# Optimization experiments

Hardware: AMD Instinct MI355X
Metric: run time of the kernel (lower is better)

The kernel has to match this reference:

```python
import jax, jax.numpy as jnp
import numpy as np

N = 32768          # total nodes
B = 64             # graphs
NPG = N // B       # nodes per graph (equal-sized graphs)
E = 524288         # edges (before self-loops)
D_IN, HID, HEADS, D_OUT = 128, 64, 4, 128
DH = HID * HEADS   # 256
NEG_SLOPE = 0.2
EPS = 1e-5

def _leaky(x):
    return jnp.where(x >= 0, x, NEG_SLOPE * x)

def gat_conv(x, src, dst, W, a_src, a_dst, b, concat):
    """PyG-style GATConv (self-loops already included in src/dst)."""
    H, C = a_src.shape
    h = (x @ W).reshape(N, H, C)                       # [N,H,C]
    es = jnp.einsum('nhc,hc->nh', h, a_src)            # score from source feats
    ed = jnp.einsum('nhc,hc->nh', h, a_dst)            # score from target feats
    e = _leaky(es[src] + ed[dst])                      # [E',H]
    m = jax.ops.segment_max(e, dst, num_segments=N)    # stable softmax per dst
    p = jnp.exp(e - m[dst])
    s = jax.ops.segment_sum(p, dst, num_segments=N)
    alpha = p / s[dst]                                 # [E',H]
    out = jax.ops.segment_sum(h[src] * alpha[..., None], dst, num_segments=N)
    out = out.reshape(N, H * C) if concat else out.mean(axis=1)
    return out + b

def mha(x, Wi, bi, Wo, bo, heads):
    """torch.nn.MultiheadAttention (batch_first, no mask, eval)."""
    Bb, T, D = x.shape
    qkv = x @ Wi.T + bi                                # [B,T,3D]
    q, k, v = jnp.split(qkv, 3, axis=-1)
    hd = D // heads
    def sp(t):
        return t.reshape(Bb, T, heads, hd).transpose(0, 2, 1, 3)  # [B,h,T,hd]
    q, k, v = sp(q), sp(k), sp(v)
    scores = jnp.einsum('bhqd,bhkd->bhqk', q, k) / jnp.sqrt(jnp.float32(hd))
    attn = jax.nn.softmax(scores, axis=-1)
    o = jnp.einsum('bhqk,bhkd->bhqd', attn, v)
    o = o.transpose(0, 2, 1, 3).reshape(Bb, T, D)
    return o @ Wo.T + bo

def layer_norm(x, g, b):
    mu = x.mean(-1, keepdims=True)
    var = x.var(-1, keepdims=True)
    return (x - mu) / jnp.sqrt(var + EPS) * g + b

def setup_inputs() -> dict:
    key = jax.random.key(0)
    ks = jax.random.split(key, 20)
    s = 0.1
    inp = {
        'x': jax.random.normal(ks[0], (N, D_IN), jnp.float32),
        'edge_index': jax.random.randint(ks[1], (2, E), 0, N, jnp.int64),
        'batch': (jnp.arange(N, dtype=jnp.int64) // NPG),
        # gat1: D_IN -> HEADS*HID (concat)
        'W1': jax.random.normal(ks[2], (D_IN, HEADS * HID), jnp.float32) * s,
        'aS1': jax.random.normal(ks[3], (HEADS, HID), jnp.float32) * s,
        'aD1': jax.random.normal(ks[4], (HEADS, HID), jnp.float32) * s,
        'b1': jnp.zeros((HEADS * HID,), jnp.float32),
        # gat2: DH -> HEADS*HID (concat)
        'W2': jax.random.normal(ks[5], (DH, HEADS * HID), jnp.float32) * s,
        'aS2': jax.random.normal(ks[6], (HEADS, HID), jnp.float32) * s,
        'aD2': jax.random.normal(ks[7], (HEADS, HID), jnp.float32) * s,
        'b2': jnp.zeros((HEADS * HID,), jnp.float32),
        # gat3: DH -> D_OUT, heads=1, concat=False (mean)
        'W3': jax.random.normal(ks[8], (DH, D_OUT), jnp.float32) * s,
        'aS3': jax.random.normal(ks[9], (1, D_OUT), jnp.float32) * s,
        'aD3': jax.random.normal(ks[10], (1, D_OUT), jnp.float32) * s,
        'b3': jnp.zeros((D_OUT,), jnp.float32),
        # MultiheadAttention
        'Wi': jax.random.normal(ks[11], (3 * DH, DH), jnp.float32) * s,
        'bi': jnp.zeros((3 * DH,), jnp.float32),
        'Wo': jax.random.normal(ks[12], (DH, DH), jnp.float32) * s,
        'bo': jnp.zeros((DH,), jnp.float32),
        # LayerNorm
        'gamma': jnp.ones((DH,), jnp.float32),
        'beta': jnp.zeros((DH,), jnp.float32),
    }
    return inp

def reference(x, edge_index, batch, W1, aS1, aD1, b1, W2, aS2, aD2, b2,
              W3, aS3, aD3, b3, Wi, bi, Wo, bo, gamma, beta):
    # add self-loops (PyG GATConv default)
    loops = jnp.arange(N, dtype=edge_index.dtype)
    src = jnp.concatenate([edge_index[0], loops])
    dst = jnp.concatenate([edge_index[1], loops])

    x1 = jax.nn.elu(gat_conv(x, src, dst, W1, aS1, aD1, b1, concat=True))
    x2 = jax.nn.elu(gat_conv(x1, src, dst, W2, aS2, aD2, b2, concat=True))

    # ragged-to-dense batching: batch = arange(N)//NPG (equal-sized, sorted),
    # so the torch python loop reduces to a reshape with no padding.
    x2b = x2.reshape(B, NPG, DH)
    attended = mha(x2b, Wi, bi, Wo, bo, HEADS).reshape(N, DH)

    x2a = layer_norm(attended + x2, gamma, beta)
    x3 = gat_conv(x2a, src, dst, W3, aS3, aD3, b3, concat=False)
    return x3
```

## Files before the change

kernel.cpp:

```cpp
#include <hip/hip_runtime.h>

typedef _Float16 half_t;
typedef _Float16 half8  __attribute__((ext_vector_type(8)));
typedef _Float16 half4v __attribute__((ext_vector_type(4)));
typedef _Float16 half2v __attribute__((ext_vector_type(2)));
typedef float    f32x4  __attribute__((ext_vector_type(4)));
typedef float    f32x2  __attribute__((ext_vector_type(2)));

constexpr int N_NODES = 32768;
constexpr int NPG_    = 512;

#define MFMA16(a, b, c) __builtin_amdgcn_mfma_f32_16x16x32_f16((a), (b), (c), 0, 0, 0)

#if defined(__has_builtin)
#  if __has_builtin(__builtin_amdgcn_cvt_pk_f16_fp8)
#    define HAVE_PK_F16_FP8 1
#  else
#    define HAVE_PK_F16_FP8 0
#  endif
#else
#  define HAVE_PK_F16_FP8 0
#endif

__device__ __forceinline__ void gload_lds16(const half_t* g, half_t* l) {
  __builtin_amdgcn_global_load_lds(
      (const __attribute__((address_space(1))) void*)g,
      (__attribute__((address_space(3))) void*)l, 16, 0, 0);
}

__device__ __forceinline__ void fp8x4_fma(int wrd, half2v p, half2v* acc) {
#if HAVE_PK_F16_FP8
  half2v lo = __builtin_amdgcn_cvt_pk_f16_fp8((short)(wrd & 0xffff));
  half2v hi = __builtin_amdgcn_cvt_pk_f16_fp8((short)(((unsigned)wrd) >> 16));
#else
  f32x2 flo = __builtin_amdgcn_cvt_pk_f32_fp8(wrd, false);
  f32x2 fhi = __builtin_amdgcn_cvt_pk_f32_fp8(wrd, true);
  half2v lo = {(half_t)flo.x, (half_t)flo.y};
  half2v hi = {(half_t)fhi.x, (half_t)fhi.y};
#endif
  acc[0] += p * lo;
  acc[1] += p * hi;
}

__global__ void k_hist(const int* __restrict__ dst, int* __restrict__ deg, int E) {
  int i = blockIdx.x * 256 + threadIdx.x;
  if (i < E) atomicAdd(&deg[dst[i]], 1);
}

__global__ __launch_bounds__(256) void k_scan1(const int* __restrict__ deg,
                                               int* __restrict__ partial,
                                               int* __restrict__ blockSums) {
  __shared__ int sd[256];
  int t = threadIdx.x;
  int i = blockIdx.x * 256 + t;
  int v = deg[i];
  sd[t] = v;
  __syncthreads();
  int acc = v;
  for (int off = 1; off < 256; off <<= 1) {
    int add = (t >= off) ? sd[t - off] : 0;
    __syncthreads();
    acc += add;
    sd[t] = acc;
    __syncthreads();
  }
  partial[i] = acc - v;
  if (t == 255) blockSums[blockIdx.x] = acc;
}

__global__ __launch_bounds__(128) void k_scan2(const int* __restrict__ blockSums,
                                               int* __restrict__ blockOff,
                                               int* __restrict__ rowptr) {
  __shared__ int sd[128];
  int t = threadIdx.x;
  int v = blockSums[t];
  sd[t] = v;
  __syncthreads();
  for (int off = 1; off < 128; off <<= 1) {
    int add = (t >= off) ? sd[t - off] : 0;
    __syncthreads();
    sd[t] += add;
    __syncthreads();
  }
  blockOff[t] = sd[t] - v;
  if (t == 127) rowptr[N_NODES] = sd[t];
}

__global__ __launch_bounds__(256) void k_scan3(const int* __restrict__ partial,
                                               const int* __restrict__ blockOff,
                                               int* __restrict__ rowptr,
                                               int* __restrict__ fill,
                                               int* __restrict__ col) {
  int i = blockIdx.x * 256 + threadIdx.x;
  int rp = partial[i] + blockOff[blockIdx.x];
  rowptr[i] = rp;
  fill[i] = 1;
  col[rp] = i;
}

__global__ void k_scatter(const int* __restrict__ src, const int* __restrict__ dst,
                          const int* __restrict__ rowptr, int* __restrict__ fill,
                          int* __restrict__ col, int E) {
  int i = blockIdx.x * 256 + threadIdx.x;
  if (i < E) {
    int d = dst[i];
    int pos = rowptr[d] + atomicAdd(&fill[d], 1);
    col[pos] = src[i];
  }
}

__global__ void k_convert(
    const float* __restrict__ x,  half_t* __restrict__ x_h,
    const float* __restrict__ W1, half_t* __restrict__ W1t,
    const float* __restrict__ W2, half_t* __restrict__ W2t,
    const float* __restrict__ W3, half_t* __restrict__ W3t,
    const float* __restrict__ Wi, half_t* __restrict__ Wi_h,
    const float* __restrict__ Wo, half_t* __restrict__ Wo_h,
    int* __restrict__ deg)
{
  int bid = blockIdx.x, t = threadIdx.x;
  if (bid < 16384) {
    int i = bid * 256 + t;
    x_h[i] = (half_t)x[i];
  } else if (bid < 16512) {
    int i = (bid - 16384) * 256 + t;
    int o = i >> 7, k = i & 127;
    W1t[i] = (half_t)W1[k * 256 + o];
  } else if (bid < 16768) {
    int i = (bid - 16512) * 256 + t;
    int o = i >> 8, k = i & 255;
    W2t[i] = (half_t)W2[k * 256 + o];
  } else if (bid < 16896) {
    int i = (bid - 16768) * 256 + t;
    int o = i >> 8, k = i & 255;
    W3t[i] = (half_t)W3[k * 128 + o];
  } else if (bid < 17664) {
    int i = (bid - 16896) * 256 + t;
    Wi_h[i] = (half_t)Wi[i];
  } else if (bid < 17920) {
    int i = (bid - 17664) * 256 + t;
    Wo_h[i] = (half_t)Wo[i];
  } else {
    deg[(bid - 17920) * 256 + t] = 1;
  }
}

__device__ __forceinline__ void gemm_wide_body(
    int bx, int by,
    const half_t* __restrict__ A, const half_t* __restrict__ Bt,
    const float* __restrict__ bias, int bias_per_row,
    half_t* __restrict__ outh, int Nc, int K,
    half_t* As, half_t* Bs)
{
  int w = threadIdx.x >> 6, lane = threadIdx.x & 63;
  int r = lane & 15, q = lane >> 4;
  int m0 = by * 128, n0 = bx * 64;
  int mh = (w & 1) * 64, nh = (w >> 1) * 32;
  f32x4 acc[4][2];
  #pragma unroll
  for (int i = 0; i < 4; i++)
    #pragma unroll
    for (int j = 0; j < 2; j++) acc[i][j] = f32x4{0.f, 0.f, 0.f, 0.f};

  int srow = lane >> 3, sc = lane & 7;

  for (int k0 = 0; k0 < K; k0 += 64) {
    __syncthreads();
    #pragma unroll
    for (int i = 0; i < 4; i++) {
      int R0 = w * 32 + i * 8;
      int row = R0 + srow;
      int cg = sc ^ (row & 7);
      gload_lds16(A + (size_t)(m0 + row) * K + k0 + cg * 8, &As[R0 * 64]);
    }
    #pragma unroll
    for (int i = 0; i < 2; i++) {
      int R0 = w * 16 + i * 8;
      int row = R0 + srow;
      int cg = sc ^ (row & 7);
      gload_lds16(Bt + (size_t)(n0 + row) * K + k0 + cg * 8, &Bs[R0 * 64]);
    }
    __syncthreads();
    #pragma unroll
    for (int kk = 0; kk < 2; kk++) {
      half8 af[4], bf[2];
      #pragma unroll
      for (int t = 0; t < 4; t++) {
        int rr = mh + t * 16 + r;
        af[t] = *(const half8*)&As[rr * 64 + (((kk * 4 + q) ^ (rr & 7)) << 3)];
      }
      #pragma unroll
      for (int t = 0; t < 2; t++) {
        int rr = nh + t * 16 + r;
        bf[t] = *(const half8*)&Bs[rr * 64 + (((kk * 4 + q) ^ (rr & 7)) << 3)];
      }
      #pragma unroll
      for (int ti = 0; ti < 4; ti++)
        #pragma unroll
        for (int tj = 0; tj < 2; tj++)
          acc[ti][tj] = MFMA16(af[ti], bf[tj], acc[ti][tj]);
    }
  }

  #pragma unroll
  for (int tj = 0; tj < 2; tj++) {
    int colc = n0 + nh + tj * 16 + r;
    float bc = bias_per_row ? 0.f : bias[colc];
    #pragma unroll
    for (int ti = 0; ti < 4; ti++) {
      #pragma unroll
      for (int i = 0; i < 4; i++) {
        int row = m0 + mh + ti * 16 + q * 4 + i;
        float bv = bias_per_row ? bias[row] : bc;
        outh[(size_t)row * Nc + colc] = (half_t)(acc[ti][tj][i] + bv);
      }
    }
  }
}

__global__ __launch_bounds__(256) void k_gemm_qkv2(
    const half_t* __restrict__ x2, const half_t* __restrict__ Wi_h,
    const float* __restrict__ bi,
    half_t* __restrict__ qk, half_t* __restrict__ vt)
{
  __shared__ __align__(16) half_t As[128 * 64];
  __shared__ __align__(16) half_t Bs[64 * 64];
  int id = blockIdx.x;
  if (id < 2048) {
    gemm_wide_body(id & 7, id >> 3, x2, Wi_h, bi, 0, qk, 512, 256, As, Bs);
  } else {
    int id2 = id - 2048;
    gemm_wide_body(id2 & 511, id2 >> 9, Wi_h + 512 * 256, x2, bi + 512, 1,
                   vt, 32768, 256, As, Bs);
  }
}

template<int NC, int H, bool FP8O>
__global__ __launch_bounds__(256) void k_gemm_gat(
    const half_t* __restrict__ A, const half_t* __restrict__ Bt,
    half_t* __restrict__ outh, unsigned char* __restrict__ out8, int K,
    const float* __restrict__ aS, const float* __restrict__ aD,
    float* __restrict__ es, float* __restrict__ ed)
{
  __shared__ __align__(16) half_t As[128 * 64];
  __shared__ __align__(16) half_t Bs[64 * 64];
  __shared__ float sRed[2][4][64];
  int w = threadIdx.x >> 6, lane = threadIdx.x & 63;
  int cc = lane & 15, qq = lane >> 4;
  int m0 = blockIdx.y * 128, n0 = blockIdx.x * 64;
  int mh = (w & 1) * 64, nh = (w >> 1) * 32;
  f32x4 acc[4][2];
  #pragma unroll
  for (int i = 0; i < 4; i++)
    #pragma unroll
    for (int j = 0; j < 2; j++) acc[i][j] = f32x4{0.f, 0.f, 0.f, 0.f};

  int srow = lane >> 3, sc = lane & 7;

  for (int k0 = 0; k0 < K; k0 += 64) {
    __syncthreads();
    #pragma unroll
    for (int i = 0; i < 4; i++) {
      int R0 = w * 32 + i * 8;
      int row = R0 + srow;
      int cg = sc ^ (row & 7);
      gload_lds16(A + (size_t)(m0 + row) * K + k0 + cg * 8, &As[R0 * 64]);
    }
    #pragma unroll
    for (int i = 0; i < 2; i++) {
      int R0 = w * 16 + i * 8;
      int row = R0 + srow;
      int cg = sc ^ (row & 7);
      gload_lds16(Bt + (size_t)(n0 + row) * K + k0 + cg * 8, &Bs[R0 * 64]);
    }
    __syncthreads();
    #pragma unroll
    for (int kk = 0; kk < 2; kk++) {
      half8 af[4], bf[2];
      #pragma unroll
      for (int t = 0; t < 4; t++) {
        int rr = mh + t * 16 + cc;
        af[t] = *(const half8*)&As[rr * 64 + (((kk * 4 + qq) ^ (rr & 7)) << 3)];
      }
      #pragma unroll
      for (int t = 0; t < 2; t++) {
        int rr = nh + t * 16 + cc;
        bf[t] = *(const half8*)&Bs[rr * 64 + (((kk * 4 + qq) ^ (rr & 7)) << 3)];
      }
      #pragma unroll
      for (int ti = 0; ti < 4; ti++)
        #pragma unroll
        for (int tj = 0; tj < 2; tj++)
          acc[ti][tj] = MFMA16(af[ti], bf[tj], acc[ti][tj]);
    }
  }

  float aSv[2], aDv[2];
  #pragma unroll
  for (int tj = 0; tj < 2; tj++) {
    int colg = n0 + nh + tj * 16 + cc;
    aSv[tj] = aS[colg];
    aDv[tj] = aD[colg];
  }
  #pragma unroll
  for (int ti = 0; ti < 4; ti++) {
    #pragma unroll
    for (int i = 0; i < 4; i++) {
      int rloc = mh + ti * 16 + qq * 4 + i;
      float ps = 0.f, pd = 0.f;
      #pragma unroll
      for (int tj = 0; tj < 2; tj++) {
        int colg = n0 + nh + tj * 16 + cc;
        float v = acc[ti][tj][i];
        if (FP8O) {
          int pk = __builtin_amdgcn_cvt_pk_fp8_f32(v, v, 0, false);
          out8[(size_t)(m0 + rloc) * NC + colg] = (unsigned char)pk;
        } else {
          outh[(size_t)(m0 + rloc) * NC + colg] = (half_t)v;
        }
        ps += v * aSv[tj];
        pd += v * aDv[tj];
      }
      #pragma unroll
      for (int off = 1; off < 16; off <<= 1) {
        ps += __shfl_xor(ps, off);
        pd += __shfl_xor(pd, off);
      }
      if (cc == 0) {
        sRed[0][w][ti * 16 + qq * 4 + i] = ps;
        sRed[1][w][ti * 16 + qq * 4 + i] = pd;
      }
    }
  }
  __syncthreads();
  if (threadIdx.x < 128) {
    int row = threadIdx.x;
    int wlo = row >> 6, ri = row & 63;
    float ps = sRed[0][wlo][ri] + sRed[0][wlo + 2][ri];
    float pd = sRed[1][wlo][ri] + sRed[1][wlo + 2][ri];
    if (H == 4) {
      int head = n0 >> 6;
      es[(size_t)(m0 + row) * 4 + head] = ps;
      ed[(size_t)(m0 + row) * 4 + head] = pd;
    } else {
      atomicAdd(&es[m0 + row], ps);
      atomicAdd(&ed[m0 + row], pd);
    }
  }
}

__global__ __launch_bounds__(256) void k_gemm_ln(
    const half_t* __restrict__ A, const half_t* __restrict__ Bt,
    const float* __restrict__ bias, const half_t* __restrict__ res,
    const float* __restrict__ gamma, const float* __restrict__ beta,
    half_t* __restrict__ outh, float* __restrict__ es0, float* __restrict__ ed0)
{
  __shared__ __align__(16) half_t As[64 * 64];
  __shared__ __align__(16) half_t Bs[256 * 64];
  __shared__ float sSum[4][64], sSq[4][64];
  __shared__ float sMR[64][2];
  int w = threadIdx.x >> 6, lane = threadIdx.x & 63;
  int r = lane & 15, q = lane >> 4;
  int m0 = blockIdx.x * 64;
  int nh = w * 64;

  if (threadIdx.x < 64) es0[m0 + threadIdx.x] = 0.f;
  else if (threadIdx.x < 128) ed0[m0 + threadIdx.x - 64] = 0.f;

  f32x4 acc[4][4];
  #pragma unroll
  for (int i = 0; i < 4; i++)
    #pragma unroll
    for (int j = 0; j < 4; j++) acc[i][j] = f32x4{0.f, 0.f, 0.f, 0.f};

  int srow = lane >> 3, sc = lane & 7;

  for (int k0 = 0; k0 < 256; k0 += 64) {
    __syncthreads();
    #pragma unroll
    for (int i = 0; i < 2; i++) {
      int R0 = w * 16 + i * 8;
      int row = R0 + srow;
      int cg = sc ^ (row & 7);
      gload_lds16(A + (size_t)(m0 + row) * 256 + k0 + cg * 8, &As[R0 * 64]);
    }
    #pragma unroll
    for (int i = 0; i < 8; i++) {
      int R0 = w * 64 + i * 8;
      int row = R0 + srow;
      int cg = sc ^ (row & 7);
      gload_lds16(Bt + (size_t)row * 256 + k0 + cg * 8, &Bs[R0 * 64]);
    }
    __syncthreads();
    #pragma unroll
    for (int kk = 0; kk < 2; kk++) {
      half8 af[4], bf[4];
      #pragma unroll
      for (int t = 0; t < 4; t++) {
        int rr = t * 16 + r;
        af[t] = *(const half8*)&As[rr * 64 + (((kk * 4 + q) ^ (rr & 7)) << 3)];
      }
      #pragma unroll
      for (int t = 0; t < 4; t++) {
        int rr = nh + t * 16 + r;
        bf[t] = *(const half8*)&Bs[rr * 64 + (((kk * 4 + q) ^ (rr & 7)) << 3)];
      }
      #pragma unroll
      for (int ti = 0; ti < 4; ti++)
        #pragma unroll
        for (int tj = 0; tj < 4; tj++)
          acc[ti][tj] = MFMA16(af[ti], bf[tj], acc[ti][tj]);
    }
  }

  float gv[4], bv[4];
  #pragma unroll
  for (int tj = 0; tj < 4; tj++) {
    int col = nh + tj * 16 + r;
    gv[tj] = gamma[col];
    bv[tj] = beta[col];
  }
  #pragma unroll
  for (int ti = 0; ti < 4; ti++) {
    #pragma unroll
    for (int i = 0; i < 4; i++) {
      int row = ti * 16 + q * 4 + i;
      float s = 0.f, ss = 0.f;
      #pragma unroll
      for (int tj = 0; tj < 4; tj++) {
        int col = nh + tj * 16 + r;
        float v = acc[ti][tj][i] + bias[col]
                + (float)res[(size_t)(m0 + row) * 256 + col];
        acc[ti][tj][i] = v;
        s += v;
        ss += v * v;
      }
      #pragma unroll
      for (int off = 1; off < 16; off <<= 1) {
        s  += __shfl_xor(s, off);
        ss += __shfl_xor(ss, off);
      }
      if (r == 0) { sSum[w][row] = s; sSq[w][row] = ss; }
    }
  }
  __syncthreads();
  if (threadIdx.x < 64) {
    int row = threadIdx.x;
    float s  = sSum[0][row] + sSum[1][row] + sSum[2][row] + sSum[3][row];
    float ss = sSq[0][row] + sSq[1][row] + sSq[2][row] + sSq[3][row];
    float mean = s * (1.f / 256.f);
    float var  = ss * (1.f / 256.f) - mean * mean;
    sMR[row][0] = mean;
    sMR[row][1] = rsqrtf(var + 1e-5f);
  }
  __syncthreads();
  #pragma unroll
  for (int ti = 0; ti < 4; ti++) {
    #pragma unroll
    for (int i = 0; i < 4; i++) {
      int row = ti * 16 + q * 4 + i;
      float mean = sMR[row][0], rstd = sMR[row][1];
      #pragma unroll
      for (int tj = 0; tj < 4; tj++) {
        int col = nh + tj * 16 + r;
        outh[(size_t)(m0 + row) * 256 + col] =
            (half_t)((acc[ti][tj][i] - mean) * rstd * gv[tj] + bv[tj]);
      }
    }
  }
}

__global__ __launch_bounds__(256) void k_agg_f16(
    const half_t* __restrict__ h, const float* __restrict__ es,
    const float* __restrict__ ed, const float* __restrict__ bias,
    const int* __restrict__ rowptr, const int* __restrict__ col,
    half_t* __restrict__ outh)
{
  int lane = threadIdx.x & 63;
  int g = lane >> 4, li = lane & 15;
  int n = blockIdx.x * 4 + (threadIdx.x >> 6);
  int cbase = li * 16;
  int hl = li >> 2;
  float edn = ed[(size_t)n * 4 + hl];
  int j0 = rowptr[n], j1 = rowptr[n + 1];
  const half_t* hb = h + cbase;

  float sum0 = 0.f, sum1 = 0.f;
  half8 acc0[2], acc1[2];
  #pragma unroll
  for (int i = 0; i < 2; i++) {
    acc0[i] = half8{0, 0, 0, 0, 0, 0, 0, 0};
    acc1[i] = half8{0, 0, 0, 0, 0, 0, 0, 0};
  }
  for (int j = j0 + g; j < j1; j += 8) {
    int jb = j + 4;
    int s0 = col[j];
    int s1 = col[(jb < j1) ? jb : j];
    float e0 = es[(size_t)s0 * 4 + hl] + edn;
    e0 = fmaxf(e0, 0.2f * e0);
    float e1 = es[(size_t)s1 * 4 + hl] + edn;
    e1 = fmaxf(e1, 0.2f * e1);
    e1 = (jb < j1) ? e1 : -1e30f;
    const half_t* hp0 = hb + (size_t)s0 * 256;
    const half_t* hp1 = hb + (size_t)s1 * 256;
    float p0 = exp2f(e0 * 1.44269504f - 8.65617025f);
    float p1 = exp2f(e1 * 1.44269504f - 8.65617025f);
    sum0 += p0; sum1 += p1;
    half_t q0 = (half_t)p0, q1 = (half_t)p1;
    half8 pv0 = {q0, q0, q0, q0, q0, q0, q0, q0};
    half8 pv1 = {q1, q1, q1, q1, q1, q1, q1, q1};
    #pragma unroll
    for (int i = 0; i < 2; i++) {
      half8 v0 = *(const half8*)(hp0 + i * 8);
      half8 v1 = *(const half8*)(hp1 + i * 8);
      acc0[i] += pv0 * v0;
      acc1[i] += pv1 * v1;
    }
  }
  float sum = sum0 + sum1;
  sum += __shfl_xor(sum, 16);
  sum += __shfl_xor(sum, 32);
  float av[16];
  #pragma unroll
  for (int i = 0; i < 16; i++) {
    av[i] = (float)acc0[i >> 3][i & 7] + (float)acc1[i >> 3][i & 7];
    av[i] += __shfl_xor(av[i], 16);
    av[i] += __shfl_xor(av[i], 32);
  }
  float inv = 1.f / sum;
  if (g == 0) {
    size_t obase = (size_t)n * 256 + cbase;
    #pragma unroll
    for (int p8 = 0; p8 < 2; p8++) {
      half8 hv;
      #pragma unroll
      for (int i = 0; i < 8; i++) {
        float t = av[p8 * 8 + i] * inv + bias[cbase + p8 * 8 + i];
        t = (t > 0.f) ? t : __expf(t) - 1.f;
        hv[i] = (half_t)t;
      }
      *(half8*)(outh + obase + p8 * 8) = hv;
    }
  }
}

__global__ __launch_bounds__(256) void k_agg_fp8(
    const unsigned char* __restrict__ hq, const float* __restrict__ es,
    const float* __restrict__ ed, const float* __restrict__ bias,
    const int* __restrict__ rowptr, const int* __restrict__ col,
    half_t* __restrict__ outh)
{
  int lane = threadIdx.x & 63;
  int g = lane >> 4, li = lane & 15;
  int n = blockIdx.x * 4 + (threadIdx.x >> 6);
  int cbase = li * 16;
  int hl = li >> 2;
  float edn = ed[(size_t)n * 4 + hl];
  int j0 = rowptr[n], j1 = rowptr[n + 1];
  const unsigned char* hb = hq + cbase;

  float sum0 = 0.f, sum1 = 0.f;
  half2v a0[8], a1[8];
  #pragma unroll
  for (int i = 0; i < 8; i++) { a0[i] = half2v{0, 0}; a1[i] = half2v{0, 0}; }

  for (int j = j0 + g; j < j1; j += 8) {
    int jb = j + 4;
    int s0 = col[j];
    int s1 = col[(jb < j1) ? jb : j];
    float e0 = es[(size_t)s0 * 4 + hl] + edn;
    e0 = fmaxf(e0, 0.2f * e0);
    float e1 = es[(size_t)s1 * 4 + hl] + edn;
    e1 = fmaxf(e1, 0.2f * e1);
    e1 = (jb < j1) ? e1 : -1e30f;
    int4 d0 = *(const int4*)(hb + (size_t)s0 * 256);
    int4 d1 = *(const int4*)(hb + (size_t)s1 * 256);
    float p0 = exp2f(e0 * 1.44269504f - 8.65617025f);
    float p1 = exp2f(e1 * 1.44269504f - 8.65617025f);
    sum0 += p0; sum1 += p1;
    half_t q0 = (half_t)p0, q1 = (half_t)p1;
    half2v pv0 = {q0, q0}, pv1 = {q1, q1};
    fp8x4_fma(d0.x, pv0, &a0[0]); fp8x4_fma(d0.y, pv0, &a0[2]);
    fp8x4_fma(d0.z, pv0, &a0[4]); fp8x4_fma(d0.w, pv0, &a0[6]);
    fp8x4_fma(d1.x, pv1, &a1[0]); fp8x4_fma(d1.y, pv1, &a1[2]);
    fp8x4_fma(d1.z, pv1, &a1[4]); fp8x4_fma(d1.w, pv1, &a1[6]);
  }

  float sum = sum0 + sum1;
  sum += __shfl_xor(sum, 16);
  sum += __shfl_xor(sum, 32);
  float av[16];
  #pragma unroll
  for (int i = 0; i < 16; i++) {
    av[i] = (float)a0[i >> 1][i & 1] + (float)a1[i >> 1][i & 1];
    av[i] += __shfl_xor(av[i], 16);
    av[i] += __shfl_xor(av[i], 32);
  }
  float inv = 1.f / sum;
  if (g == 0) {
    size_t obase = (size_t)n * 256 + cbase;
    #pragma unroll
    for (int p8 = 0; p8 < 2; p8++) {
      half8 hv;
      #pragma unroll
      for (int i = 0; i < 8; i++) {
        float t = av[p8 * 8 + i] * inv + bias[cbase + p8 * 8 + i];
        t = (t > 0.f) ? t : __expf(t) - 1.f;
        hv[i] = (half_t)t;
      }
      *(half8*)(outh + obase + p8 * 8) = hv;
    }
  }
}

__global__ __launch_bounds__(256) void k_agg3(
    const half_t* __restrict__ h, const float* __restrict__ es,
    const float* __restrict__ ed, const float* __restrict__ bias,
    const int* __restrict__ rowptr, const int* __restrict__ col,
    float* __restrict__ outf)
{
  constexpr int VPT = 8;
  int lane = threadIdx.x & 63;
  int g = lane >> 4, li = lane & 15;
  int n = blockIdx.x * 4 + (threadIdx.x >> 6);
  int cbase = li * VPT;
  float edn = ed[n];
  int j0 = rowptr[n], j1 = rowptr[n + 1];
  const half_t* hb = h + cbase;

  float sum0 = 0.f, sum1 = 0.f;
  float acc0[VPT], acc1[VPT];
  #pragma unroll
  for (int i = 0; i < VPT; i++) { acc0[i] = 0.f; acc1[i] = 0.f; }
  for (int j = j0 + g; j < j1; j += 8) {
    int jb = j + 4;
    int s0 = col[j];
    int s1 = col[(jb < j1) ? jb : j];
    float e0 = es[s0] + edn;
    e0 = fmaxf(e0, 0.2f * e0);
    float e1 = es[s1] + edn;
    e1 = fmaxf(e1, 0.2f * e1);
    e1 = (jb < j1) ? e1 : -1e30f;
    const half_t* hp0 = hb + (size_t)s0 * 128;
    const half_t* hp1 = hb + (size_t)s1 * 128;
    float p0 = __expf(e0), p1 = __expf(e1);
    sum0 += p0; sum1 += p1;
    half8 v0 = *(const half8*)hp0;
    half8 v1 = *(const half8*)hp1;
    #pragma unroll
    for (int i = 0; i < 8; i++) {
      acc0[i] += p0 * (float)v0[i];
      acc1[i] += p1 * (float)v1[i];
    }
  }
  float sum = sum0 + sum1;
  sum += __shfl_xor(sum, 16);
  sum += __shfl_xor(sum, 32);
  float av[VPT];
  #pragma unroll
  for (int i = 0; i < VPT; i++) {
    av[i] = acc0[i] + acc1[i];
    av[i] += __shfl_xor(av[i], 16);
    av[i] += __shfl_xor(av[i], 32);
  }
  float inv = 1.f / sum;
  if (g == 0) {
    size_t obase = (size_t)n * 128 + cbase;
    #pragma unroll
    for (int p4 = 0; p4 < 2; p4++) {
      float4 fv = {av[p4 * 4] * inv + bias[cbase + p4 * 4],
                   av[p4 * 4 + 1] * inv + bias[cbase + p4 * 4 + 1],
                   av[p4 * 4 + 2] * inv + bias[cbase + p4 * 4 + 2],
                   av[p4 * 4 + 3] * inv + bias[cbase + p4 * 4 + 3]};
      *(float4*)(outf + obase + p4 * 4) = fv;
    }
  }
}

__global__ __launch_bounds__(256) void k_attn(
    const half_t* __restrict__ qk, const half_t* __restrict__ vt,
    half_t* __restrict__ o)
{
  __shared__ __align__(16) half_t Kt[64 * 64];
  __shared__ __align__(16) half_t Vt[64 * 64];
  __shared__ __align__(16) half_t Pb[4][16][72];

  int pair = blockIdx.x;
  int b = pair >> 2, hh = pair & 3;
  int q0 = blockIdx.y * 64;
  int w = threadIdx.x >> 6, lane = threadIdx.x & 63;
  int cc = lane & 15, qq = lane >> 4;

  const half_t* Qp = qk + ((size_t)(b * NPG_ + q0 + w * 16 + cc) * 512 + hh * 64);
  half8 qa0 = *(const half8*)(Qp + qq * 8);
  half8 qa1 = *(const half8*)(Qp + 32 + qq * 8);

  f32x4 oacc[4];
  #pragma unroll
  for (int t = 0; t < 4; t++) oacc[t] = f32x4{0.f, 0.f, 0.f, 0.f};
  float rs = 0.f;

  const half_t* kb = qk + ((size_t)(b * NPG_) * 512 + 256 + hh * 64);
  const half_t* vb = vt + ((size_t)(hh * 64) * 32768 + b * NPG_);

  int krow = lane >> 3, ksl = lane & 7;

  for (int kt = 0; kt < 8; kt++) {
    __syncthreads();
    #pragma unroll
    for (int i = 0; i < 2; i++) {
      int R = w * 16 + i * 8;
      int kr = R + krow;
      gload_lds16(kb + (size_t)(kt * 64 + kr) * 512 + ((ksl ^ (kr & 7)) * 8),
                  &Kt[R * 64]);
      gload_lds16(vb + (size_t)kr * 32768 + kt * 64 + ((ksl ^ (kr & 7)) * 8),
                  &Vt[R * 64]);
    }
    __syncthreads();

    #pragma unroll
    for (int mt = 0; mt < 4; mt++) {
      int key = mt * 16 + cc;
      half8 k0 = *(const half8*)&Kt[key * 64 + ((qq ^ (key & 7)) << 3)];
      half8 k1 = *(const half8*)&Kt[key * 64 + (((qq + 4) ^ (key & 7)) << 3)];
      f32x4 s = f32x4{0.f, 0.f, 0.f, 0.f};
      s = MFMA16(k0, qa0, s);
      s = MFMA16(k1, qa1, s);
      half4v ph;
      #pragma unroll
      for (int i = 0; i < 4; i++) {
        float p = exp2f(s[i] * 0.180336886f - 11.54156033f);
        rs += p;
        ph[i] = (half_t)p;
      }
      *(half4v*)&Pb[w][cc][mt * 16 + qq * 4] = ph;
    }

    #pragma unroll
    for (int kc = 0; kc < 2; kc++) {
      half8 a = *(const half8*)&Pb[w][cc][kc * 32 + qq * 8];
      #pragma unroll
      for (int nt = 0; nt < 4; nt++) {
        int d = nt * 16 + cc;
        half8 bb = *(const half8*)&Vt[d * 64 + (((kc * 4 + qq) ^ (d & 7)) << 3)];
        oacc[nt] = MFMA16(a, bb, oacc[nt]);
      }
    }
  }

  rs += __shfl_xor(rs, 16);
  rs += __shfl_xor(rs, 32);
  #pragma unroll
  for (int i = 0; i < 4; i++) {
    float rsv = __shfl(rs, qq * 4 + i);
    float inv = 1.f / rsv;
    int node = b * NPG_ + q0 + w * 16 + qq * 4 + i;
    #pragma unroll
    for (int nt = 0; nt < 4; nt++)
      o[(size_t)node * 256 + hh * 64 + nt * 16 + cc] = (half_t)(oacc[nt][i] * inv);
  }
}

extern "C" void kernel_launch(void* const* d_in, const int* in_sizes, int n_in,
                              void* d_out, int out_size, void* d_ws, size_t ws_size,
                              hipStream_t stream)
{
  const float* x    = (const float*)d_in[0];
  const int*   ei   = (const int*)d_in[1];
  const float* W1   = (const float*)d_in[3];
  const float* aS1  = (const float*)d_in[4];
  const float* aD1  = (const float*)d_in[5];
  const float* b1   = (const float*)d_in[6];
  const float* W2   = (const float*)d_in[7];
  const float* aS2  = (const float*)d_in[8];
  const float* aD2  = (const float*)d_in[9];
  const float* b2   = (const float*)d_in[10];
  const float* W3   = (const float*)d_in[11];
  const float* aS3  = (const float*)d_in[12];
  const float* aD3  = (const float*)d_in[13];
  const float* b3   = (const float*)d_in[14];
  const float* Wi   = (const float*)d_in[15];
  const float* bi   = (const float*)d_in[16];
  const float* Wo   = (const float*)d_in[17];
  const float* bo   = (const float*)d_in[18];
  const float* gam  = (const float*)d_in[19];
  const float* bet  = (const float*)d_in[20];
  float* out = (float*)d_out;
  const int N = N_NODES;
  int E = in_sizes[1] / 2;

  char* ws = (char*)d_ws;
  size_t off = 0;
  auto alloc = [&](size_t bytes) -> void* {
    void* p = ws + off;
    off = (off + bytes + 255) & ~(size_t)255;
    return p;
  };
  half_t* x_h    = (half_t*)alloc((size_t)N * 128 * 2);
  half_t* h_h    = (half_t*)alloc((size_t)N * 256 * 2);
  unsigned char* hq = (unsigned char*)alloc((size_t)N * 256);
  half_t* x1_h   = (half_t*)alloc((size_t)N * 256 * 2);
  half_t* x2_h   = (half_t*)alloc((size_t)N * 256 * 2);
  half_t* qk_h   = (half_t*)alloc((size_t)N * 512 * 2);
  half_t* vt_h   = (half_t*)alloc((size_t)256 * N * 2);
  half_t* o_h    = (half_t*)alloc((size_t)N * 256 * 2);
  half_t* x2a_h  = (half_t*)alloc((size_t)N * 256 * 2);
  half_t* W1t    = (half_t*)alloc(256 * 128 * 2);
  half_t* W2t    = (half_t*)alloc(256 * 256 * 2);
  half_t* W3t    = (half_t*)alloc(128 * 256 * 2);
  half_t* Wi_h   = (half_t*)alloc(768 * 256 * 2);
  half_t* Wo_h   = (half_t*)alloc(256 * 256 * 2);
  float*  es     = (float*) alloc((size_t)N * 4 * 4);
  float*  ed     = (float*) alloc((size_t)N * 4 * 4);
  int*    deg    = (int*)   alloc((size_t)N * 4);
  int*    fill   = (int*)   alloc((size_t)N * 4);
  int*    rowptr = (int*)   alloc(((size_t)N + 1) * 4);
  int*    col    = (int*)   alloc((size_t)(N + E) * 4);
  int*    part   = (int*)   alloc((size_t)N * 4);
  int*    bsum   = (int*)   alloc(128 * 4);
  int*    boff   = (int*)   alloc(128 * 4);

  const int* srcE = ei;
  const int* dstE = ei + E;

  k_convert<<<18048, 256, 0, stream>>>(x, x_h, W1, W1t, W2, W2t, W3, W3t,
                                       Wi, Wi_h, Wo, Wo_h, deg);
  k_hist<<<(E + 255) / 256, 256, 0, stream>>>(dstE, deg, E);
  k_scan1<<<128, 256, 0, stream>>>(deg, part, bsum);
  k_scan2<<<1, 128, 0, stream>>>(bsum, boff, rowptr);
  k_scan3<<<128, 256, 0, stream>>>(part, boff, rowptr, fill, col);
  k_scatter<<<(E + 255) / 256, 256, 0, stream>>>(srcE, dstE, rowptr, fill, col, E);

  k_gemm_gat<256, 4, false><<<dim3(4, N / 128), 256, 0, stream>>>(
      x_h, W1t, h_h, nullptr, 128, aS1, aD1, es, ed);
  k_agg_f16<<<N / 4, 256, 0, stream>>>(h_h, es, ed, b1, rowptr, col, x1_h);

  k_gemm_gat<256, 4, true><<<dim3(4, N / 128), 256, 0, stream>>>(
      x1_h, W2t, nullptr, hq, 256, aS2, aD2, es, ed);
  k_agg_fp8<<<N / 4, 256, 0, stream>>>(hq, es, ed, b2, rowptr, col, x2_h);

  k_gemm_qkv2<<<3072, 256, 0, stream>>>(x2_h, Wi_h, bi, qk_h, vt_h);
  k_attn<<<dim3(256, 8), 256, 0, stream>>>(qk_h, vt_h, o_h);

  k_gemm_ln<<<N / 64, 256, 0, stream>>>(o_h, Wo_h, bo, x2_h, gam, bet, x2a_h, es, ed);

  k_gemm_gat<128, 1, false><<<dim3(2, N / 128), 256, 0, stream>>>(
      x2a_h, W3t, h_h, nullptr, 256, aS3, aD3, es, ed);
  k_agg3<<<N / 4, 256, 0, stream>>>(h_h, es, ed, b3, rowptr, col, out);
}
```

Baseline: 393.6 us.

## Double-buffer K/V tiles in attention kernel with async prefetch and MFMA priority

The attention kernel now keeps two LDS buffers for K and V. The next key tile is prefetched with direct global-to-LDS loads while the current tile is being computed, and partial vmcnt waits with raw barriers replace the full syncthreads pair. It also raises wave priority around the MFMA sections. The goal is to hide global load latency behind compute, at the cost of twice the LDS use, which may lower occupancy. Correctness depends on the hand-written vmcnt counts matching the number of outstanding loads.

```diff
diff --git a/kernel.cpp b/kernel.cpp
--- a/kernel.cpp
+++ b/kernel.cpp
@@ -681,8 +681,8 @@
     const half_t* __restrict__ qk, const half_t* __restrict__ vt,
     half_t* __restrict__ o)
 {
-  __shared__ __align__(16) half_t Kt[64 * 64];
-  __shared__ __align__(16) half_t Vt[64 * 64];
+  __shared__ __align__(16) half_t Kt[2][64 * 64];
+  __shared__ __align__(16) half_t Vt[2][64 * 64];
   __shared__ __align__(16) half_t Pb[4][16][72];
 
   int pair = blockIdx.x;
@@ -705,27 +705,45 @@
 
   int krow = lane >> 3, ksl = lane & 7;
 
+  #pragma unroll
+  for (int i = 0; i < 2; i++) {
+    int R = w * 16 + i * 8;
+    int kr = R + krow;
+    gload_lds16(kb + (size_t)kr * 512 + ((ksl ^ (kr & 7)) * 8), &Kt[0][R * 64]);
+    gload_lds16(vb + (size_t)kr * 32768 + ((ksl ^ (kr & 7)) * 8), &Vt[0][R * 64]);
+  }
+
   for (int kt = 0; kt < 8; kt++) {
-    __syncthreads();
-    #pragma unroll
-    for (int i = 0; i < 2; i++) {
-      int R = w * 16 + i * 8;
-      int kr = R + krow;
-      gload_lds16(kb + (size_t)(kt * 64 + kr) * 512 + ((ksl ^ (kr & 7)) * 8),
-                  &Kt[R * 64]);
-      gload_lds16(vb + (size_t)kr * 32768 + kt * 64 + ((ksl ^ (kr & 7)) * 8),
-                  &Vt[R * 64]);
-    }
-    __syncthreads();
+    half_t* Kc = Kt[kt & 1];
+    half_t* Vc = Vt[kt & 1];
+    if (kt < 7) {
+      half_t* Kn = Kt[(kt & 1) ^ 1];
+      half_t* Vn = Vt[(kt & 1) ^ 1];
+      #pragma unroll
+      for (int i = 0; i < 2; i++) {
+        int R = w * 16 + i * 8;
+        int kr = R + krow;
+        gload_lds16(kb + (size_t)((kt + 1) * 64 + kr) * 512 + ((ksl ^ (kr & 7)) * 8),
+                    &Kn[R * 64]);
+        gload_lds16(vb + (size_t)kr * 32768 + (kt + 1) * 64 + ((ksl ^ (kr & 7)) * 8),
+                    &Vn[R * 64]);
+      }
+      asm volatile("s_waitcnt vmcnt(4)" ::: "memory");
+    } else {
+      asm volatile("s_waitcnt vmcnt(0)" ::: "memory");
+    }
+    __builtin_amdgcn_s_barrier();
 
     #pragma unroll
     for (int mt = 0; mt < 4; mt++) {
       int key = mt * 16 + cc;
-      half8 k0 = *(const half8*)&Kt[key * 64 + ((qq ^ (key & 7)) << 3)];
-      half8 k1 = *(const half8*)&Kt[key * 64 + (((qq + 4) ^ (key & 7)) << 3)];
+      half8 k0 = *(const half8*)&Kc[key * 64 + ((qq ^ (key & 7)) << 3)];
+      half8 k1 = *(const half8*)&Kc[key * 64 + (((qq + 4) ^ (key & 7)) << 3)];
       f32x4 s = f32x4{0.f, 0.f, 0.f, 0.f};
+      __builtin_amdgcn_s_setprio(1);
       s = MFMA16(k0, qa0, s);
       s = MFMA16(k1, qa1, s);
+      __builtin_amdgcn_s_setprio(0);
       half4v ph;
       #pragma unroll
       for (int i = 0; i < 4; i++) {
@@ -736,16 +754,20 @@
       *(half4v*)&Pb[w][cc][mt * 16 + qq * 4] = ph;
     }
 
+    __builtin_amdgcn_s_setprio(1);
     #pragma unroll
     for (int kc = 0; kc < 2; kc++) {
       half8 a = *(const half8*)&Pb[w][cc][kc * 32 + qq * 8];
       #pragma unroll
       for (int nt = 0; nt < 4; nt++) {
         int d = nt * 16 + cc;
-        half8 bb = *(const half8*)&Vt[d * 64 + (((kc * 4 + qq) ^ (d & 7)) << 3)];
+        half8 bb = *(const half8*)&Vc[d * 64 + (((kc * 4 + qq) ^ (d & 7)) << 3)];
         oacc[nt] = MFMA16(a, bb, oacc[nt]);
       }
     }
+    __builtin_amdgcn_s_setprio(0);
+
+    if (kt < 7) __builtin_amdgcn_s_barrier();
   }
 
   rs += __shfl_xor(rs, 16);
```

After: 396.4 us. No clear change (+0.7%).
